# Kernel optimization log

Measured on AMD Instinct MI355X. Metric: run time of the kernel, lower is better.

The kernel has to match this reference:

```python
import jax, jax.numpy as jnp
import numpy as np

N_NODES = 50000
N_EDGES = 600000
D_IN = 128
D_OUT = 128
LN_EPS = 1e-5
LEAKY_SLOPE = 0.2


def setup_inputs() -> dict:
    key = jax.random.key(0)
    k1, k2, k3, k4 = jax.random.split(key, 4)
    x = jax.random.normal(k1, (N_NODES, D_IN), dtype=jnp.float32)
    edge_index = jax.random.randint(k2, (2, N_EDGES), 0, N_NODES, dtype=jnp.int64)
    # xavier_uniform with gain for relu (sqrt(2))
    gain = float(np.sqrt(2.0))
    lim_w = gain * np.sqrt(6.0 / (D_IN + D_OUT))
    W_lin = jax.random.uniform(k3, (D_OUT, D_IN), minval=-lim_w, maxval=lim_w, dtype=jnp.float32)
    lim_a = gain * np.sqrt(6.0 / (2 * D_OUT + 1))
    a = jax.random.uniform(k4, (2 * D_OUT,), minval=-lim_a, maxval=lim_a, dtype=jnp.float32)
    gamma = jnp.ones((D_OUT,), dtype=jnp.float32)
    beta = jnp.zeros((D_OUT,), dtype=jnp.float32)
    return {"x": x, "edge_index": edge_index, "W_lin": W_lin, "a": a,
            "gamma": gamma, "beta": beta}


def reference(x, edge_index, W_lin, a, gamma, beta):
    N = x.shape[0]
    h = x @ W_lin.T                                  # [N, D_OUT]
    d = h.shape[1]
    # attention MLP on concat([h_src, h_dst]) == h_src@a[:d] + h_dst@a[d:]
    s_src = h @ a[:d]                                # [N]
    s_dst = h @ a[d:]                                # [N]
    src, dst = edge_index[0], edge_index[1]
    e = jax.nn.leaky_relu(s_src[src] + s_dst[dst], LEAKY_SLOPE)   # [E]
    # segment softmax over destination nodes (numerically stable)
    m = jax.ops.segment_max(e, dst, num_segments=N)               # [N], -inf for empty
    ex = jnp.exp(e - m[dst])                                      # [E]
    z = jax.ops.segment_sum(ex, dst, num_segments=N)              # [N]
    alpha = ex / z[dst]                                           # [E]
    # weighted scatter-add of source messages
    msgs = h[src] * alpha[:, None]                                # [E, D_OUT]
    agg = jax.ops.segment_sum(msgs, dst, num_segments=N)          # [N, D_OUT]
    # residual (input_dim == output_dim -> identity projection) + LayerNorm
    y = agg + x
    mu = jnp.mean(y, axis=-1, keepdims=True)
    var = jnp.mean(jnp.square(y - mu), axis=-1, keepdims=True)
    return (y - mu) * jax.lax.rsqrt(var + LN_EPS) * gamma + beta
```

## Files before the change

kernel.cpp:

```cpp
#include <hip/hip_runtime.h>
#include <hip/hip_bf16.h>

typedef unsigned short u16;
typedef unsigned int   u32;
typedef __bf16 bf16x8 __attribute__((ext_vector_type(8)));
typedef float  f32x4  __attribute__((ext_vector_type(4)));

#define D 128

__device__ inline float bflo(u32 u) { return __builtin_bit_cast(float, u << 16); }
__device__ inline float bfhi(u32 u) { return __builtin_bit_cast(float, u & 0xffff0000u); }
__device__ inline float bfu(u16 u)  { return __builtin_bit_cast(float, ((u32)u) << 16); }
__device__ inline u16 f2bf(float f) {
    __hip_bfloat16 b = __float2bfloat16(f);
    return __builtin_bit_cast(u16, b);
}

__global__ __launch_bounds__(256) void k_init(const u32* __restrict__ x32,
                                              const int* __restrict__ ei32,
                                              int* __restrict__ cnt, int N,
                                              int* __restrict__ flags)
{
    int i = blockIdx.x * 256 + threadIdx.x;
    if (i < N) cnt[i] = 0;
    if (blockIdx.x == 0 && threadIdx.x < 64) {
        int lane = threadIdx.x;
        u32 v = x32[lane];
        u32 elo = (v >> 7) & 0xFFu;
        int hits = __popcll(__ballot(elo >= 150u));
        int nz   = __popcll(__ballot(ei32[2 * lane + 1] != 0));
        if (lane == 0) {
            flags[0] = (hits >= 4) ? 1 : 0;
            flags[1] = (nz < 8) ? 1 : 0;
        }
    }
}

__global__ __launch_bounds__(256) void k_gemm(const void* __restrict__ xv,
                                              const void* __restrict__ Wv,
                                              const void* __restrict__ av,
                                              u16* __restrict__ h,
                                              float* __restrict__ s_src,
                                              float* __restrict__ s_dst, int N,
                                              const int* __restrict__ flags)
{
    const int f32  = flags[0];
    const int wave = threadIdx.x >> 6;
    const int lane = threadIdx.x & 63;
    const int quad = lane >> 4;
    const int l16  = lane & 15;
    const int m0   = blockIdx.x * 64 + wave * 16;

    int arow = m0 + l16;
    if (arow > N - 1) arow = N - 1;

    bf16x8 afrag[4];
    if (f32) {
        const float* xr = (const float*)xv + (size_t)arow * D + quad * 8;
#pragma unroll
        for (int s = 0; s < 4; ++s) {
            f32x4 v0 = *(const f32x4*)(xr + s * 32);
            f32x4 v1 = *(const f32x4*)(xr + s * 32 + 4);
            union { u16 u[8]; bf16x8 v; } t;
#pragma unroll
            for (int j = 0; j < 4; ++j) { t.u[j] = f2bf(v0[j]); t.u[4 + j] = f2bf(v1[j]); }
            afrag[s] = t.v;
        }
    } else {
        const u16* xr = (const u16*)xv + (size_t)arow * D + quad * 8;
#pragma unroll
        for (int s = 0; s < 4; ++s)
            afrag[s] = __builtin_bit_cast(bf16x8, *(const uint4*)(xr + s * 32));
    }

    f32x4 acc[8] = {};
#pragma unroll
    for (int t = 0; t < 8; ++t) {
#pragma unroll
        for (int s = 0; s < 4; ++s) {
            bf16x8 b;
            if (f32) {
                const float* wr = (const float*)Wv + (size_t)(t * 16 + l16) * D + quad * 8 + s * 32;
                f32x4 v0 = *(const f32x4*)wr;
                f32x4 v1 = *(const f32x4*)(wr + 4);
                union { u16 u[8]; bf16x8 v; } tb;
#pragma unroll
                for (int j = 0; j < 4; ++j) { tb.u[j] = f2bf(v0[j]); tb.u[4 + j] = f2bf(v1[j]); }
                b = tb.v;
            } else {
                const u16* wr = (const u16*)Wv + (size_t)(t * 16 + l16) * D + quad * 8 + s * 32;
                b = __builtin_bit_cast(bf16x8, *(const uint4*)wr);
            }
            acc[t] = __builtin_amdgcn_mfma_f32_16x16x32_bf16(afrag[s], b, acc[t], 0, 0, 0);
        }
    }

    float as[8], ad[8];
    if (f32) {
        const float* af = (const float*)av;
#pragma unroll
        for (int t = 0; t < 8; ++t) { as[t] = af[t * 16 + l16]; ad[t] = af[D + t * 16 + l16]; }
    } else {
        const u16* au = (const u16*)av;
#pragma unroll
        for (int t = 0; t < 8; ++t) { as[t] = bfu(au[t * 16 + l16]); ad[t] = bfu(au[D + t * 16 + l16]); }
    }

#pragma unroll
    for (int i = 0; i < 4; ++i) {
        int r = m0 + quad * 4 + i;
        float ps = 0.f, pd = 0.f;
#pragma unroll
        for (int t = 0; t < 8; ++t) {
            float v = acc[t][i];
            ps += v * as[t];
            pd += v * ad[t];
        }
#pragma unroll
        for (int m = 1; m < 16; m <<= 1) {
            ps += __shfl_xor(ps, m, 64);
            pd += __shfl_xor(pd, m, 64);
        }
        if (r < N) {
            if (l16 == 0) { s_src[r] = ps; s_dst[r] = pd; }
            u16* hrow = h + (size_t)r * D + l16;
#pragma unroll
            for (int t = 0; t < 8; ++t)
                hrow[t * 16] = f2bf(acc[t][i]);
        }
    }
}

__global__ __launch_bounds__(256) void k_edge(const int* __restrict__ ei,
                                              const float* __restrict__ s_src,
                                              const float* __restrict__ s_dst,
                                              int* __restrict__ cnt,
                                              u32* __restrict__ bkt, int E,
                                              const int* __restrict__ flags)
{
    int e = blockIdx.x * 256 + threadIdx.x;
    if (e >= E) return;
    int src, dst;
    if (flags[1]) {
        int2 vs = ((const int2*)ei)[e];
        int2 vd = ((const int2*)ei)[E + e];
        src = vs.x; dst = vd.x;
    } else {
        src = ei[e]; dst = ei[E + e];
    }
    float sv = s_src[src] + s_dst[dst];
    float lr = sv > 0.f ? sv : 0.2f * sv;
    float ex = __expf(lr);
    int t = atomicAdd(cnt + dst, 1);
    if (t < 64)
        bkt[dst * 64 + t] = (u32)(src & 0xFFFF) | ((u32)f2bf(ex) << 16);
}

__global__ __launch_bounds__(256) void k_agg(const u16* __restrict__ h,
                                             const void* __restrict__ xv,
                                             const int* __restrict__ cnt,
                                             const u32* __restrict__ bkt,
                                             const void* __restrict__ gv_,
                                             const void* __restrict__ bv_,
                                             void* __restrict__ outv, int N,
                                             const int* __restrict__ flags)
{
    const int f32 = flags[0];
    const int wave = threadIdx.x >> 6, lane = threadIdx.x & 63;
    const int quad = lane >> 4;
    const int l16  = lane & 15;
    const int n = blockIdx.x * 4 + wave;
    if (n >= N) return;
    int d = cnt[n]; if (d > 64) d = 64;
    const u32* slots = bkt + n * 64;

    float acc[8] = {};
    float zs = 0.f;
    int j = 0;
    for (; j + 8 <= d; j += 8) {
        u32 pk0 = slots[j + quad];
        u32 pk1 = slots[j + 4 + quad];
        uint4 hv0 = *(const uint4*)(h + (size_t)(pk0 & 0xFFFF) * D + l16 * 8);
        uint4 hv1 = *(const uint4*)(h + (size_t)(pk1 & 0xFFFF) * D + l16 * 8);
        float w0 = bfhi(pk0), w1 = bfhi(pk1);
        zs += w0 + w1;
        acc[0] += w0 * bflo(hv0.x); acc[1] += w0 * bfhi(hv0.x);
        acc[2] += w0 * bflo(hv0.y); acc[3] += w0 * bfhi(hv0.y);
        acc[4] += w0 * bflo(hv0.z); acc[5] += w0 * bfhi(hv0.z);
        acc[6] += w0 * bflo(hv0.w); acc[7] += w0 * bfhi(hv0.w);
        acc[0] += w1 * bflo(hv1.x); acc[1] += w1 * bfhi(hv1.x);
        acc[2] += w1 * bflo(hv1.y); acc[3] += w1 * bfhi(hv1.y);
        acc[4] += w1 * bflo(hv1.z); acc[5] += w1 * bfhi(hv1.z);
        acc[6] += w1 * bflo(hv1.w); acc[7] += w1 * bfhi(hv1.w);
    }
    for (; j + 4 <= d; j += 4) {
        u32 pk = slots[j + quad];
        float w = bfhi(pk);
        uint4 hv = *(const uint4*)(h + (size_t)(pk & 0xFFFF) * D + l16 * 8);
        zs += w;
        acc[0] += w * bflo(hv.x); acc[1] += w * bfhi(hv.x);
        acc[2] += w * bflo(hv.y); acc[3] += w * bfhi(hv.y);
        acc[4] += w * bflo(hv.z); acc[5] += w * bfhi(hv.z);
        acc[6] += w * bflo(hv.w); acc[7] += w * bfhi(hv.w);
    }
    if (j + quad < d) {
        u32 pk = slots[j + quad];
        float w = bfhi(pk);
        uint4 hv = *(const uint4*)(h + (size_t)(pk & 0xFFFF) * D + l16 * 8);
        zs += w;
        acc[0] += w * bflo(hv.x); acc[1] += w * bfhi(hv.x);
        acc[2] += w * bflo(hv.y); acc[3] += w * bfhi(hv.y);
        acc[4] += w * bflo(hv.z); acc[5] += w * bfhi(hv.z);
        acc[6] += w * bflo(hv.w); acc[7] += w * bfhi(hv.w);
    }
#pragma unroll
    for (int k = 0; k < 8; ++k) {
        acc[k] += __shfl_xor(acc[k], 16, 64);
        acc[k] += __shfl_xor(acc[k], 32, 64);
    }
    zs += __shfl_xor(zs, 16, 64);
    zs += __shfl_xor(zs, 32, 64);
    float inv = d > 0 ? 1.f / zs : 0.f;

    float y[8], g[8], bb[8];
    if (f32) {
        const float* xr = (const float*)xv + (size_t)n * D + l16 * 8;
        const float* gr = (const float*)gv_ + l16 * 8;
        const float* br = (const float*)bv_ + l16 * 8;
#pragma unroll
        for (int k = 0; k < 8; ++k) { y[k] = acc[k] * inv + xr[k]; g[k] = gr[k]; bb[k] = br[k]; }
    } else {
        uint4 xr = *(const uint4*)((const u16*)xv + (size_t)n * D + l16 * 8);
        uint4 gr = *(const uint4*)((const u16*)gv_ + l16 * 8);
        uint4 br = *(const uint4*)((const u16*)bv_ + l16 * 8);
        const u32 xw[4] = {xr.x, xr.y, xr.z, xr.w};
        const u32 gw[4] = {gr.x, gr.y, gr.z, gr.w};
        const u32 bw[4] = {br.x, br.y, br.z, br.w};
#pragma unroll
        for (int k = 0; k < 4; ++k) {
            y[2*k]   = acc[2*k]   * inv + bflo(xw[k]);
            y[2*k+1] = acc[2*k+1] * inv + bfhi(xw[k]);
            g[2*k] = bflo(gw[k]); g[2*k+1] = bfhi(gw[k]);
            bb[2*k] = bflo(bw[k]); bb[2*k+1] = bfhi(bw[k]);
        }
    }
    float s1 = 0.f, s2 = 0.f;
#pragma unroll
    for (int k = 0; k < 8; ++k) { s1 += y[k]; s2 += y[k] * y[k]; }
#pragma unroll
    for (int m = 1; m < 16; m <<= 1) {
        s1 += __shfl_xor(s1, m, 64);
        s2 += __shfl_xor(s2, m, 64);
    }
    float mu  = s1 * (1.f / 128.f);
    float var = s2 * (1.f / 128.f) - mu * mu;
    float r   = rsqrtf(var + 1e-5f);

    if (quad == 0) {
        if (f32) {
            float* orow = (float*)outv + (size_t)n * D + l16 * 8;
            f32x4 o0, o1;
#pragma unroll
            for (int k = 0; k < 4; ++k) o0[k] = (y[k] - mu) * r * g[k] + bb[k];
#pragma unroll
            for (int k = 0; k < 4; ++k) o1[k] = (y[4+k] - mu) * r * g[4+k] + bb[4+k];
            *(f32x4*)orow = o0;
            *(f32x4*)(orow + 4) = o1;
        } else {
            uint4 pk;
            u32 w[4];
#pragma unroll
            for (int k = 0; k < 4; ++k) {
                float o0 = (y[2*k]   - mu) * r * g[2*k]   + bb[2*k];
                float o1 = (y[2*k+1] - mu) * r * g[2*k+1] + bb[2*k+1];
                w[k] = (u32)f2bf(o0) | ((u32)f2bf(o1) << 16);
            }
            pk.x = w[0]; pk.y = w[1]; pk.z = w[2]; pk.w = w[3];
            *(uint4*)((u16*)outv + (size_t)n * D + l16 * 8) = pk;
        }
    }
}

extern "C" void kernel_launch(void* const* d_in, const int* in_sizes, int n_in,
                              void* d_out, int out_size, void* d_ws, size_t ws_size,
                              hipStream_t stream)
{
    const void* x  = d_in[0];
    const int*  ei = (const int*)d_in[1];
    const void* W  = d_in[2];
    const void* a  = d_in[3];
    const void* gm = d_in[4];
    const void* bt = d_in[5];

    const int N = in_sizes[0] / D;
    const int E = in_sizes[1] / 2;

    char* ws = (char*)d_ws;
    size_t off = 0;
    u16*   h     = (u16*)(ws + off);   off += (size_t)N * D * sizeof(u16);
    float* ssrc  = (float*)(ws + off); off += (size_t)N * sizeof(float);
    float* sdst  = (float*)(ws + off); off += (size_t)N * sizeof(float);
    int*   cnt   = (int*)(ws + off);   off += (size_t)N * sizeof(int);
    int*   flags = (int*)(ws + off);   off += 256;
    u32*   bkt   = (u32*)(ws + off);   off += (size_t)N * 64 * sizeof(u32);

    k_init <<<(N + 255) / 256, 256, 0, stream>>>((const u32*)x, ei, cnt, N, flags);
    k_gemm <<<(N + 63) / 64,   256, 0, stream>>>(x, W, a, h, ssrc, sdst, N, flags);
    k_edge <<<(E + 255) / 256, 256, 0, stream>>>(ei, ssrc, sdst, cnt, bkt, E, flags);
    k_agg  <<<(N + 3) / 4,     256, 0, stream>>>(h, x, cnt, bkt, gm, bt, d_out, N, flags);
}
```

Before: 182.2 us.

## Fuse init, GEMM, edge, and aggregation kernels into one cooperative persistent kernel

Replaces the four separate kernel launches with a single cooperative kernel that runs the GEMM, edge scoring and aggregation phases in grid-stride loops, separated by grid-wide syncs. Type detection now happens in every block instead of through a flags buffer. The goal is to remove launch overhead and inter-kernel gaps. In exchange it adds grid.sync costs, limits the grid to the resident block count, and adds host-side occupancy and device queries on every launch.

```diff
diff --git a/kernel.cpp b/kernel.cpp
--- a/kernel.cpp
+++ b/kernel.cpp
@@ -1,5 +1,8 @@
 #include <hip/hip_runtime.h>
 #include <hip/hip_bf16.h>
+#include <hip/hip_cooperative_groups.h>
+
+namespace cg = cooperative_groups;
 
 typedef unsigned short u16;
 typedef unsigned int   u32;
@@ -16,267 +19,255 @@
     return __builtin_bit_cast(u16, b);
 }
 
-__global__ __launch_bounds__(256) void k_init(const u32* __restrict__ x32,
-                                              const int* __restrict__ ei32,
-                                              int* __restrict__ cnt, int N,
-                                              int* __restrict__ flags)
+__device__ inline void detect(const u32* __restrict__ x32, const int* __restrict__ ei32,
+                              int& f32, int& i64)
 {
-    int i = blockIdx.x * 256 + threadIdx.x;
-    if (i < N) cnt[i] = 0;
-    if (blockIdx.x == 0 && threadIdx.x < 64) {
-        int lane = threadIdx.x;
-        u32 v = x32[lane];
-        u32 elo = (v >> 7) & 0xFFu;
-        int hits = __popcll(__ballot(elo >= 150u));
-        int nz   = __popcll(__ballot(ei32[2 * lane + 1] != 0));
-        if (lane == 0) {
-            flags[0] = (hits >= 4) ? 1 : 0;
-            flags[1] = (nz < 8) ? 1 : 0;
+    int lane = threadIdx.x & 63;
+    u32 v = x32[lane];
+    u32 elo = (v >> 7) & 0xFFu;
+    int hits = __popcll(__ballot(elo >= 150u));
+    int nz   = __popcll(__ballot(ei32[2 * lane + 1] != 0));
+    f32 = (hits >= 4);
+    i64 = (nz < 8);
+}
+
+__global__ __launch_bounds__(256, 4) void k_fused(
+    const void* __restrict__ xv, const int* __restrict__ ei,
+    const void* __restrict__ Wv, const void* __restrict__ av,
+    const void* __restrict__ gv_, const void* __restrict__ bv_,
+    void* __restrict__ outv,
+    u16* __restrict__ h, float* __restrict__ s_src, float* __restrict__ s_dst,
+    int* __restrict__ cnt, u32* __restrict__ bkt, int N, int E)
+{
+    cg::grid_group grid = cg::this_grid();
+
+    int f32, i64;
+    detect((const u32*)xv, ei, f32, i64);
+
+    const int tid   = threadIdx.x;
+    const int nblk  = gridDim.x;
+    const int wave  = tid >> 6;
+    const int lane  = tid & 63;
+    const int quad  = lane >> 4;
+    const int l16   = lane & 15;
+
+    for (int i = blockIdx.x * 256 + tid; i < N; i += nblk * 256)
+        cnt[i] = 0;
+
+    const int T = (N + 63) / 64;
+    for (int t0 = blockIdx.x; t0 < T; t0 += nblk) {
+        const int m0 = t0 * 64 + wave * 16;
+        int arow = m0 + l16;
+        if (arow > N - 1) arow = N - 1;
+
+        bf16x8 afrag[4];
+        if (f32) {
+            const float* xr = (const float*)xv + (size_t)arow * D + quad * 8;
+#pragma unroll
+            for (int s = 0; s < 4; ++s) {
+                f32x4 v0 = *(const f32x4*)(xr + s * 32);
+                f32x4 v1 = *(const f32x4*)(xr + s * 32 + 4);
+                union { u16 u[8]; bf16x8 v; } t;
+#pragma unroll
+                for (int j = 0; j < 4; ++j) { t.u[j] = f2bf(v0[j]); t.u[4 + j] = f2bf(v1[j]); }
+                afrag[s] = t.v;
+            }
+        } else {
+            const u16* xr = (const u16*)xv + (size_t)arow * D + quad * 8;
+#pragma unroll
+            for (int s = 0; s < 4; ++s)
+                afrag[s] = __builtin_bit_cast(bf16x8, *(const uint4*)(xr + s * 32));
+        }
+
+        f32x4 acc[8] = {};
+#pragma unroll
+        for (int t = 0; t < 8; ++t) {
+#pragma unroll
+            for (int s = 0; s < 4; ++s) {
+                bf16x8 b;
+                if (f32) {
+                    const float* wr = (const float*)Wv + (size_t)(t * 16 + l16) * D + quad * 8 + s * 32;
+                    f32x4 v0 = *(const f32x4*)wr;
+                    f32x4 v1 = *(const f32x4*)(wr + 4);
+                    union { u16 u[8]; bf16x8 v; } tb;
+#pragma unroll
+                    for (int j = 0; j < 4; ++j) { tb.u[j] = f2bf(v0[j]); tb.u[4 + j] = f2bf(v1[j]); }
+                    b = tb.v;
+                } else {
+                    const u16* wr = (const u16*)Wv + (size_t)(t * 16 + l16) * D + quad * 8 + s * 32;
+                    b = __builtin_bit_cast(bf16x8, *(const uint4*)wr);
+                }
+                acc[t] = __builtin_amdgcn_mfma_f32_16x16x32_bf16(afrag[s], b, acc[t], 0, 0, 0);
+            }
+        }
+
+        float as[8], ad[8];
+        if (f32) {
+            const float* af = (const float*)av;
+#pragma unroll
+            for (int t = 0; t < 8; ++t) { as[t] = af[t * 16 + l16]; ad[t] = af[D + t * 16 + l16]; }
+        } else {
+            const u16* au = (const u16*)av;
+#pragma unroll
+            for (int t = 0; t < 8; ++t) { as[t] = bfu(au[t * 16 + l16]); ad[t] = bfu(au[D + t * 16 + l16]); }
+        }
+
+#pragma unroll
+        for (int i = 0; i < 4; ++i) {
+            int r = m0 + quad * 4 + i;
+            float ps = 0.f, pd = 0.f;
+#pragma unroll
+            for (int t = 0; t < 8; ++t) {
+                float v = acc[t][i];
+                ps += v * as[t];
+                pd += v * ad[t];
+            }
+#pragma unroll
+            for (int m = 1; m < 16; m <<= 1) {
+                ps += __shfl_xor(ps, m, 64);
+                pd += __shfl_xor(pd, m, 64);
+            }
+            if (r < N) {
+                if (l16 == 0) { s_src[r] = ps; s_dst[r] = pd; }
+                u16* hrow = h + (size_t)r * D + l16;
+#pragma unroll
+                for (int t = 0; t < 8; ++t)
+                    hrow[t * 16] = f2bf(acc[t][i]);
+            }
         }
     }
-}
-
-__global__ __launch_bounds__(256) void k_gemm(const void* __restrict__ xv,
-                                              const void* __restrict__ Wv,
-                                              const void* __restrict__ av,
-                                              u16* __restrict__ h,
-                                              float* __restrict__ s_src,
-                                              float* __restrict__ s_dst, int N,
-                                              const int* __restrict__ flags)
-{
-    const int f32  = flags[0];
-    const int wave = threadIdx.x >> 6;
-    const int lane = threadIdx.x & 63;
-    const int quad = lane >> 4;
-    const int l16  = lane & 15;
-    const int m0   = blockIdx.x * 64 + wave * 16;
-
-    int arow = m0 + l16;
-    if (arow > N - 1) arow = N - 1;
-
-    bf16x8 afrag[4];
-    if (f32) {
-        const float* xr = (const float*)xv + (size_t)arow * D + quad * 8;
-#pragma unroll
-        for (int s = 0; s < 4; ++s) {
-            f32x4 v0 = *(const f32x4*)(xr + s * 32);
-            f32x4 v1 = *(const f32x4*)(xr + s * 32 + 4);
-            union { u16 u[8]; bf16x8 v; } t;
-#pragma unroll
-            for (int j = 0; j < 4; ++j) { t.u[j] = f2bf(v0[j]); t.u[4 + j] = f2bf(v1[j]); }
-            afrag[s] = t.v;
-        }
-    } else {
-        const u16* xr = (const u16*)xv + (size_t)arow * D + quad * 8;
-#pragma unroll
-        for (int s = 0; s < 4; ++s)
-            afrag[s] = __builtin_bit_cast(bf16x8, *(const uint4*)(xr + s * 32));
+
+    grid.sync();
+
+    for (int e = blockIdx.x * 256 + tid; e < E; e += nblk * 256) {
+        int src, dst;
+        if (i64) {
+            int2 vs = ((const int2*)ei)[e];
+            int2 vd = ((const int2*)ei)[E + e];
+            src = vs.x; dst = vd.x;
+        } else {
+            src = ei[e]; dst = ei[E + e];
+        }
+        float sv = s_src[src] + s_dst[dst];
+        float lr = sv > 0.f ? sv : 0.2f * sv;
+        float ex = __expf(lr);
+        int t = atomicAdd(cnt + dst, 1);
+        if (t < 64)
+            bkt[dst * 64 + t] = (u32)(src & 0xFFFF) | ((u32)f2bf(ex) << 16);
     }
 
-    f32x4 acc[8] = {};
-#pragma unroll
-    for (int t = 0; t < 8; ++t) {
-#pragma unroll
-        for (int s = 0; s < 4; ++s) {
-            bf16x8 b;
+    grid.sync();
+
+    for (int n0 = blockIdx.x * 4; n0 < N; n0 += nblk * 4) {
+        const int n = n0 + wave;
+        if (n >= N) continue;
+        int d = cnt[n]; if (d > 64) d = 64;
+        const u32* slots = bkt + n * 64;
+
+        float acc[8] = {};
+        float zs = 0.f;
+        int j = 0;
+        for (; j + 8 <= d; j += 8) {
+            u32 pk0 = slots[j + quad];
+            u32 pk1 = slots[j + 4 + quad];
+            uint4 hv0 = *(const uint4*)(h + (size_t)(pk0 & 0xFFFF) * D + l16 * 8);
+            uint4 hv1 = *(const uint4*)(h + (size_t)(pk1 & 0xFFFF) * D + l16 * 8);
+            float w0 = bfhi(pk0), w1 = bfhi(pk1);
+            zs += w0 + w1;
+            acc[0] += w0 * bflo(hv0.x); acc[1] += w0 * bfhi(hv0.x);
+            acc[2] += w0 * bflo(hv0.y); acc[3] += w0 * bfhi(hv0.y);
+            acc[4] += w0 * bflo(hv0.z); acc[5] += w0 * bfhi(hv0.z);
+            acc[6] += w0 * bflo(hv0.w); acc[7] += w0 * bfhi(hv0.w);
+            acc[0] += w1 * bflo(hv1.x); acc[1] += w1 * bfhi(hv1.x);
+            acc[2] += w1 * bflo(hv1.y); acc[3] += w1 * bfhi(hv1.y);
+            acc[4] += w1 * bflo(hv1.z); acc[5] += w1 * bfhi(hv1.z);
+            acc[6] += w1 * bflo(hv1.w); acc[7] += w1 * bfhi(hv1.w);
+        }
+        for (; j + 4 <= d; j += 4) {
+            u32 pk = slots[j + quad];
+            float w = bfhi(pk);
+            uint4 hv = *(const uint4*)(h + (size_t)(pk & 0xFFFF) * D + l16 * 8);
+            zs += w;
+            acc[0] += w * bflo(hv.x); acc[1] += w * bfhi(hv.x);
+            acc[2] += w * bflo(hv.y); acc[3] += w * bfhi(hv.y);
+            acc[4] += w * bflo(hv.z); acc[5] += w * bfhi(hv.z);
+            acc[6] += w * bflo(hv.w); acc[7] += w * bfhi(hv.w);
+        }
+        if (j + quad < d) {
+            u32 pk = slots[j + quad];
+            float w = bfhi(pk);
+            uint4 hv = *(const uint4*)(h + (size_t)(pk & 0xFFFF) * D + l16 * 8);
+            zs += w;
+            acc[0] += w * bflo(hv.x); acc[1] += w * bfhi(hv.x);
+            acc[2] += w * bflo(hv.y); acc[3] += w * bfhi(hv.y);
+            acc[4] += w * bflo(hv.z); acc[5] += w * bfhi(hv.z);
+            acc[6] += w * bflo(hv.w); acc[7] += w * bfhi(hv.w);
+        }
+#pragma unroll
+        for (int k = 0; k < 8; ++k) {
+            acc[k] += __shfl_xor(acc[k], 16, 64);
+            acc[k] += __shfl_xor(acc[k], 32, 64);
+        }
+        zs += __shfl_xor(zs, 16, 64);
+        zs += __shfl_xor(zs, 32, 64);
+        float inv = d > 0 ? 1.f / zs : 0.f;
+
+        float y[8], g[8], bb[8];
+        if (f32) {
+            const float* xr = (const float*)xv + (size_t)n * D + l16 * 8;
+            const float* gr = (const float*)gv_ + l16 * 8;
+            const float* br = (const float*)bv_ + l16 * 8;
+#pragma unroll
+            for (int k = 0; k < 8; ++k) { y[k] = acc[k] * inv + xr[k]; g[k] = gr[k]; bb[k] = br[k]; }
+        } else {
+            uint4 xr = *(const uint4*)((const u16*)xv + (size_t)n * D + l16 * 8);
+            uint4 gr = *(const uint4*)((const u16*)gv_ + l16 * 8);
+            uint4 br = *(const uint4*)((const u16*)bv_ + l16 * 8);
+            const u32 xw[4] = {xr.x, xr.y, xr.z, xr.w};
+            const u32 gw[4] = {gr.x, gr.y, gr.z, gr.w};
+            const u32 bw[4] = {br.x, br.y, br.z, br.w};
+#pragma unroll
+            for (int k = 0; k < 4; ++k) {
+                y[2*k]   = acc[2*k]   * inv + bflo(xw[k]);
+                y[2*k+1] = acc[2*k+1] * inv + bfhi(xw[k]);
+                g[2*k] = bflo(gw[k]); g[2*k+1] = bfhi(gw[k]);
+                bb[2*k] = bflo(bw[k]); bb[2*k+1] = bfhi(bw[k]);
+            }
+        }
+        float s1 = 0.f, s2 = 0.f;
+#pragma unroll
+        for (int k = 0; k < 8; ++k) { s1 += y[k]; s2 += y[k] * y[k]; }
+#pragma unroll
+        for (int m = 1; m < 16; m <<= 1) {
+            s1 += __shfl_xor(s1, m, 64);
+            s2 += __shfl_xor(s2, m, 64);
+        }
+        float mu  = s1 * (1.f / 128.f);
+        float var = s2 * (1.f / 128.f) - mu * mu;
+        float r   = rsqrtf(var + 1e-5f);
+
+        if (quad == 0) {
             if (f32) {
-                const float* wr = (const float*)Wv + (size_t)(t * 16 + l16) * D + quad * 8 + s * 32;
-                f32x4 v0 = *(const f32x4*)wr;
-                f32x4 v1 = *(const f32x4*)(wr + 4);
-                union { u16 u[8]; bf16x8 v; } tb;
-#pragma unroll
-                for (int j = 0; j < 4; ++j) { tb.u[j] = f2bf(v0[j]); tb.u[4 + j] = f2bf(v1[j]); }
-                b = tb.v;
+                float* orow = (float*)outv + (size_t)n * D + l16 * 8;
+                f32x4 o0, o1;
+#pragma unroll
+                for (int k = 0; k < 4; ++k) o0[k] = (y[k] - mu) * r * g[k] + bb[k];
+#pragma unroll
+                for (int k = 0; k < 4; ++k) o1[k] = (y[4+k] - mu) * r * g[4+k] + bb[4+k];
+                *(f32x4*)orow = o0;
+                *(f32x4*)(orow + 4) = o1;
             } else {
-                const u16* wr = (const u16*)Wv + (size_t)(t * 16 + l16) * D + quad * 8 + s * 32;
-                b = __builtin_bit_cast(bf16x8, *(const uint4*)wr);
-            }
-            acc[t] = __builtin_amdgcn_mfma_f32_16x16x32_bf16(afrag[s], b, acc[t], 0, 0, 0);
-        }
-    }
-
-    float as[8], ad[8];
-    if (f32) {
-        const float* af = (const float*)av;
-#pragma unroll
-        for (int t = 0; t < 8; ++t) { as[t] = af[t * 16 + l16]; ad[t] = af[D + t * 16 + l16]; }
-    } else {
-        const u16* au = (const u16*)av;
-#pragma unroll
-        for (int t = 0; t < 8; ++t) { as[t] = bfu(au[t * 16 + l16]); ad[t] = bfu(au[D + t * 16 + l16]); }
-    }
-
-#pragma unroll
-    for (int i = 0; i < 4; ++i) {
-        int r = m0 + quad * 4 + i;
-        float ps = 0.f, pd = 0.f;
-#pragma unroll
-        for (int t = 0; t < 8; ++t) {
-            float v = acc[t][i];
-            ps += v * as[t];
-            pd += v * ad[t];
-        }
-#pragma unroll
-        for (int m = 1; m < 16; m <<= 1) {
-            ps += __shfl_xor(ps, m, 64);
-            pd += __shfl_xor(pd, m, 64);
-        }
-        if (r < N) {
-            if (l16 == 0) { s_src[r] = ps; s_dst[r] = pd; }
-            u16* hrow = h + (size_t)r * D + l16;
-#pragma unroll
-            for (int t = 0; t < 8; ++t)
-                hrow[t * 16] = f2bf(acc[t][i]);
-        }
-    }
-}
-
-__global__ __launch_bounds__(256) void k_edge(const int* __restrict__ ei,
-                                              const float* __restrict__ s_src,
-                                              const float* __restrict__ s_dst,
-                                              int* __restrict__ cnt,
-                                              u32* __restrict__ bkt, int E,
-                                              const int* __restrict__ flags)
-{
-    int e = blockIdx.x * 256 + threadIdx.x;
-    if (e >= E) return;
-    int src, dst;
-    if (flags[1]) {
-        int2 vs = ((const int2*)ei)[e];
-        int2 vd = ((const int2*)ei)[E + e];
-        src = vs.x; dst = vd.x;
-    } else {
-        src = ei[e]; dst = ei[E + e];
-    }
-    float sv = s_src[src] + s_dst[dst];
-    float lr = sv > 0.f ? sv : 0.2f * sv;
-    float ex = __expf(lr);
-    int t = atomicAdd(cnt + dst, 1);
-    if (t < 64)
-        bkt[dst * 64 + t] = (u32)(src & 0xFFFF) | ((u32)f2bf(ex) << 16);
-}
-
-__global__ __launch_bounds__(256) void k_agg(const u16* __restrict__ h,
-                                             const void* __restrict__ xv,
-                                             const int* __restrict__ cnt,
-                                             const u32* __restrict__ bkt,
-                                             const void* __restrict__ gv_,
-                                             const void* __restrict__ bv_,
-                                             void* __restrict__ outv, int N,
-                                             const int* __restrict__ flags)
-{
-    const int f32 = flags[0];
-    const int wave = threadIdx.x >> 6, lane = threadIdx.x & 63;
-    const int quad = lane >> 4;
-    const int l16  = lane & 15;
-    const int n = blockIdx.x * 4 + wave;
-    if (n >= N) return;
-    int d = cnt[n]; if (d > 64) d = 64;
-    const u32* slots = bkt + n * 64;
-
-    float acc[8] = {};
-    float zs = 0.f;
-    int j = 0;
-    for (; j + 8 <= d; j += 8) {
-        u32 pk0 = slots[j + quad];
-        u32 pk1 = slots[j + 4 + quad];
-        uint4 hv0 = *(const uint4*)(h + (size_t)(pk0 & 0xFFFF) * D + l16 * 8);
-        uint4 hv1 = *(const uint4*)(h + (size_t)(pk1 & 0xFFFF) * D + l16 * 8);
-        float w0 = bfhi(pk0), w1 = bfhi(pk1);
-        zs += w0 + w1;
-        acc[0] += w0 * bflo(hv0.x); acc[1] += w0 * bfhi(hv0.x);
-        acc[2] += w0 * bflo(hv0.y); acc[3] += w0 * bfhi(hv0.y);
-        acc[4] += w0 * bflo(hv0.z); acc[5] += w0 * bfhi(hv0.z);
-        acc[6] += w0 * bflo(hv0.w); acc[7] += w0 * bfhi(hv0.w);
-        acc[0] += w1 * bflo(hv1.x); acc[1] += w1 * bfhi(hv1.x);
-        acc[2] += w1 * bflo(hv1.y); acc[3] += w1 * bfhi(hv1.y);
-        acc[4] += w1 * bflo(hv1.z); acc[5] += w1 * bfhi(hv1.z);
-        acc[6] += w1 * bflo(hv1.w); acc[7] += w1 * bfhi(hv1.w);
-    }
-    for (; j + 4 <= d; j += 4) {
-        u32 pk = slots[j + quad];
-        float w = bfhi(pk);
-        uint4 hv = *(const uint4*)(h + (size_t)(pk & 0xFFFF) * D + l16 * 8);
-        zs += w;
-        acc[0] += w * bflo(hv.x); acc[1] += w * bfhi(hv.x);
-        acc[2] += w * bflo(hv.y); acc[3] += w * bfhi(hv.y);
-        acc[4] += w * bflo(hv.z); acc[5] += w * bfhi(hv.z);
-        acc[6] += w * bflo(hv.w); acc[7] += w * bfhi(hv.w);
-    }
-    if (j + quad < d) {
-        u32 pk = slots[j + quad];
-        float w = bfhi(pk);
-        uint4 hv = *(const uint4*)(h + (size_t)(pk & 0xFFFF) * D + l16 * 8);
-        zs += w;
-        acc[0] += w * bflo(hv.x); acc[1] += w * bfhi(hv.x);
-        acc[2] += w * bflo(hv.y); acc[3] += w * bfhi(hv.y);
-        acc[4] += w * bflo(hv.z); acc[5] += w * bfhi(hv.z);
-        acc[6] += w * bflo(hv.w); acc[7] += w * bfhi(hv.w);
-    }
-#pragma unroll
-    for (int k = 0; k < 8; ++k) {
-        acc[k] += __shfl_xor(acc[k], 16, 64);
-        acc[k] += __shfl_xor(acc[k], 32, 64);
-    }
-    zs += __shfl_xor(zs, 16, 64);
-    zs += __shfl_xor(zs, 32, 64);
-    float inv = d > 0 ? 1.f / zs : 0.f;
-
-    float y[8], g[8], bb[8];
-    if (f32) {
-        const float* xr = (const float*)xv + (size_t)n * D + l16 * 8;
-        const float* gr = (const float*)gv_ + l16 * 8;
-        const float* br = (const float*)bv_ + l16 * 8;
-#pragma unroll
-        for (int k = 0; k < 8; ++k) { y[k] = acc[k] * inv + xr[k]; g[k] = gr[k]; bb[k] = br[k]; }
-    } else {
-        uint4 xr = *(const uint4*)((const u16*)xv + (size_t)n * D + l16 * 8);
-        uint4 gr = *(const uint4*)((const u16*)gv_ + l16 * 8);
-        uint4 br = *(const uint4*)((const u16*)bv_ + l16 * 8);
-        const u32 xw[4] = {xr.x, xr.y, xr.z, xr.w};
-        const u32 gw[4] = {gr.x, gr.y, gr.z, gr.w};
-        const u32 bw[4] = {br.x, br.y, br.z, br.w};
-#pragma unroll
-        for (int k = 0; k < 4; ++k) {
-            y[2*k]   = acc[2*k]   * inv + bflo(xw[k]);
-            y[2*k+1] = acc[2*k+1] * inv + bfhi(xw[k]);
-            g[2*k] = bflo(gw[k]); g[2*k+1] = bfhi(gw[k]);
-            bb[2*k] = bflo(bw[k]); bb[2*k+1] = bfhi(bw[k]);
-        }
-    }
-    float s1 = 0.f, s2 = 0.f;
-#pragma unroll
-    for (int k = 0; k < 8; ++k) { s1 += y[k]; s2 += y[k] * y[k]; }
-#pragma unroll
-    for (int m = 1; m < 16; m <<= 1) {
-        s1 += __shfl_xor(s1, m, 64);
-        s2 += __shfl_xor(s2, m, 64);
-    }
-    float mu  = s1 * (1.f / 128.f);
-    float var = s2 * (1.f / 128.f) - mu * mu;
-    float r   = rsqrtf(var + 1e-5f);
-
-    if (quad == 0) {
-        if (f32) {
-            float* orow = (float*)outv + (size_t)n * D + l16 * 8;
-            f32x4 o0, o1;
-#pragma unroll
-            for (int k = 0; k < 4; ++k) o0[k] = (y[k] - mu) * r * g[k] + bb[k];
-#pragma unroll
-            for (int k = 0; k < 4; ++k) o1[k] = (y[4+k] - mu) * r * g[4+k] + bb[4+k];
-            *(f32x4*)orow = o0;
-            *(f32x4*)(orow + 4) = o1;
-        } else {
-            uint4 pk;
-            u32 w[4];
-#pragma unroll
-            for (int k = 0; k < 4; ++k) {
-                float o0 = (y[2*k]   - mu) * r * g[2*k]   + bb[2*k];
-                float o1 = (y[2*k+1] - mu) * r * g[2*k+1] + bb[2*k+1];
-                w[k] = (u32)f2bf(o0) | ((u32)f2bf(o1) << 16);
-            }
-            pk.x = w[0]; pk.y = w[1]; pk.z = w[2]; pk.w = w[3];
-            *(uint4*)((u16*)outv + (size_t)n * D + l16 * 8) = pk;
+                uint4 pk;
+                u32 w[4];
+#pragma unroll
+                for (int k = 0; k < 4; ++k) {
+                    float o0 = (y[2*k]   - mu) * r * g[2*k]   + bb[2*k];
+                    float o1 = (y[2*k+1] - mu) * r * g[2*k+1] + bb[2*k+1];
+                    w[k] = (u32)f2bf(o0) | ((u32)f2bf(o1) << 16);
+                }
+                pk.x = w[0]; pk.y = w[1]; pk.z = w[2]; pk.w = w[3];
+                *(uint4*)((u16*)outv + (size_t)n * D + l16 * 8) = pk;
+            }
         }
     }
 }
@@ -291,21 +282,30 @@
     const void* a  = d_in[3];
     const void* gm = d_in[4];
     const void* bt = d_in[5];
-
-    const int N = in_sizes[0] / D;
-    const int E = in_sizes[1] / 2;
+    void* out = d_out;
+
+    int N = in_sizes[0] / D;
+    int E = in_sizes[1] / 2;
 
     char* ws = (char*)d_ws;
     size_t off = 0;
-    u16*   h     = (u16*)(ws + off);   off += (size_t)N * D * sizeof(u16);
-    float* ssrc  = (float*)(ws + off); off += (size_t)N * sizeof(float);
-    float* sdst  = (float*)(ws + off); off += (size_t)N * sizeof(float);
-    int*   cnt   = (int*)(ws + off);   off += (size_t)N * sizeof(int);
-    int*   flags = (int*)(ws + off);   off += 256;
-    u32*   bkt   = (u32*)(ws + off);   off += (size_t)N * 64 * sizeof(u32);
-
-    k_init <<<(N + 255) / 256, 256, 0, stream>>>((const u32*)x, ei, cnt, N, flags);
-    k_gemm <<<(N + 63) / 64,   256, 0, stream>>>(x, W, a, h, ssrc, sdst, N, flags);
-    k_edge <<<(E + 255) / 256, 256, 0, stream>>>(ei, ssrc, sdst, cnt, bkt, E, flags);
-    k_agg  <<<(N + 3) / 4,     256, 0, stream>>>(h, x, cnt, bkt, gm, bt, d_out, N, flags);
+    u16*   h    = (u16*)(ws + off);   off += (size_t)N * D * sizeof(u16);
+    float* ssrc = (float*)(ws + off); off += (size_t)N * sizeof(float);
+    float* sdst = (float*)(ws + off); off += (size_t)N * sizeof(float);
+    int*   cnt  = (int*)(ws + off);   off += (size_t)N * sizeof(int);
+    u32*   bkt  = (u32*)(ws + off);   off += (size_t)N * 64 * sizeof(u32);
+
+    int dev = 0; hipGetDevice(&dev);
+    int cus = 256;
+    hipDeviceGetAttribute(&cus, hipDeviceAttributeMultiprocessorCount, dev);
+    int bpc = 1;
+    hipOccupancyMaxActiveBlocksPerMultiprocessor(&bpc, k_fused, 256, 0);
+    if (bpc < 1) bpc = 1;
+    int grid = cus * bpc;
+
+    void* args[] = { (void*)&x, (void*)&ei, (void*)&W, (void*)&a, (void*)&gm, (void*)&bt,
+                     (void*)&out, (void*)&h, (void*)&ssrc, (void*)&sdst,
+                     (void*)&cnt, (void*)&bkt, (void*)&N, (void*)&E };
+    hipLaunchCooperativeKernel((const void*)k_fused, dim3(grid), dim3(256),
+                               args, 0, stream);
 }
```

Result: slower. 364.8 us (+100.2%).
